# Kernel tuning notes

Measured on AMD Instinct MI355X. Metric: run time of the kernel, lower is better.

The kernel has to match this reference:

```python
import jax, jax.numpy as jnp
import numpy as np
import math

N_HEADS = 16
ROPE_THETA = 10000.0
NEG_INF = -1e30


def setup_inputs() -> dict:
    key = jax.random.key(0)
    k1, k2, k3, k4 = jax.random.split(key, 4)
    B, S, D = 2, 2048, 2048
    x = jax.random.normal(k1, (B, S, D), dtype=jnp.float32)
    qkv = 0.01 * jax.random.normal(k2, (2 * D, D), dtype=jnp.float32)
    H = N_HEADS
    dh = D // H
    nope = dh // 2
    rope = dh // 2
    wk = 0.01 * jax.random.normal(k3, (H * nope + rope, D), dtype=jnp.float32)
    wo = 0.01 * jax.random.normal(k4, (D, D), dtype=jnp.float32)
    return {"x": x, "qkv": qkv, "wk": wk, "wo": wo}


def _rope_cos_sin(S, dh, rope_dim, dtype):
    # freqs over full dh as in the torch module, then sliced to rope_dim//2 and tiled x2
    freqs = 1.0 / (ROPE_THETA ** (jnp.arange(0, dh, 2).astype(jnp.float32) / dh))
    emb = jnp.arange(S, dtype=jnp.float32)[:, None] * freqs[None, :]  # [S, dh//2]
    cos = jnp.tile(jnp.cos(emb)[:, : rope_dim // 2], (1, 2))[None, None]  # [1,1,S,rope]
    sin = jnp.tile(jnp.sin(emb)[:, : rope_dim // 2], (1, 2))[None, None]
    return cos.astype(dtype), sin.astype(dtype)


def _apply_rope(xq, cos, sin):
    x1, x2 = jnp.split(xq, 2, axis=-1)
    return xq * cos + jnp.concatenate([-x2, x1], axis=-1) * sin


def reference(x, qkv, wk, wo):
    B, S, D = x.shape
    H = N_HEADS
    dh = D // H
    nope = dh // 2
    rope = dh // 2

    QV = x @ qkv.T                              # [B,S,2D]
    Q, V = jnp.split(QV, 2, axis=-1)
    Q = Q.reshape(B, S, H, dh).transpose(0, 2, 1, 3)        # [B,H,S,dh]
    v_heads = V.reshape(B, S, H, dh).transpose(0, 2, 1, 3)  # [B,H,S,dh]
    Qn, Qr = Q[..., :nope], Q[..., nope:]

    K = x @ wk.T                                # [B,S,H*nope+rope]
    Kn = K[..., : H * nope].reshape(B, S, H, nope).transpose(0, 2, 1, 3)  # [B,H,S,nope]
    Kr = K[..., H * nope :].reshape(B, S, 1, rope).transpose(0, 2, 1, 3)  # [B,1,S,rope]

    cos, sin = _rope_cos_sin(S, dh, rope, x.dtype)
    Qr = _apply_rope(Qr, cos, sin)
    Kr = _apply_rope(Kr, cos, sin)

    q_heads = jnp.concatenate([Qn, Qr], axis=-1)                               # [B,H,S,dh]
    k_heads = jnp.concatenate([Kn, jnp.broadcast_to(Kr, (B, H, S, rope))], -1)  # [B,H,S,dh]

    scale = 1.0 / math.sqrt(dh)
    scores = jnp.einsum('bhqd,bhkd->bhqk', q_heads, k_heads) * scale
    mask = jnp.tril(jnp.ones((S, S), dtype=bool))
    scores = jnp.where(mask[None, None], scores, NEG_INF)
    attn = jax.nn.softmax(scores, axis=-1)
    out = jnp.einsum('bhqk,bhkd->bhqd', attn, v_heads)
    out = out.transpose(0, 2, 1, 3).reshape(B, S, D) @ wo.T
    return (out, k_heads, v_heads)
```

## Files before the change

### kernel.cpp

```cpp
#include <hip/hip_runtime.h>
#include <hip/hip_bf16.h>


typedef unsigned short u16;
typedef unsigned int u32;
typedef __bf16 bf16x8 __attribute__((ext_vector_type(8)));
typedef float f32x4 __attribute__((ext_vector_type(4)));
typedef float f32x16 __attribute__((ext_vector_type(16)));

__device__ __forceinline__ u16 f2bf(float x) {
  union { __hip_bfloat16 h; u16 u; } c;
  c.h = __float2bfloat16(x);
  return c.u;
}
__device__ __forceinline__ float bf2f(u16 u) {
  union { u32 u; float f; } c;
  c.u = ((u32)u) << 16;
  return c.f;
}
__device__ __forceinline__ u32 pack2(float a, float b) {
  return (u32)f2bf(a) | ((u32)f2bf(b) << 16);
}
__device__ __forceinline__ f32x4 mfma16(bf16x8 a, bf16x8 b, f32x4 c) {
  return __builtin_amdgcn_mfma_f32_16x16x32_bf16(a, b, c, 0, 0, 0);
}
__device__ __forceinline__ f32x16 mfma32(bf16x8 a, bf16x8 b, f32x16 c) {
  return __builtin_amdgcn_mfma_f32_32x32x16_bf16(a, b, c, 0, 0, 0);
}
__device__ __forceinline__ void gload_lds16(const void* g, void* l) {
  __builtin_amdgcn_global_load_lds((__attribute__((address_space(1))) void*)g,
                                   (__attribute__((address_space(3))) void*)l,
                                   16, 0, 0);
}

__global__ __launch_bounds__(256) void cast_all(const float4* __restrict__ x,
                                                const float4* __restrict__ qkv,
                                                const float* __restrict__ wk,
                                                const float4* __restrict__ wo,
                                                u16* __restrict__ x_bf,
                                                u16* __restrict__ wcomb,
                                                u16* __restrict__ wo_bf) {
  int i = blockIdx.x * blockDim.x + threadIdx.x;
  const float4* src;
  u16* dst;
  int j;
  if (i < 2097152) {
    src = x; dst = x_bf; j = i;
  } else if (i < 4194304) {
    src = qkv; dst = wcomb; j = i - 2097152;
  } else if (i < 4849664) {
    j = i - 4194304;
    int r = (j * 4) >> 11;
    u32 lo = 0, hi = 0;
    if (r < 1088) {
      float4 v = ((const float4*)wk)[j];
      lo = pack2(v.x, v.y);
      hi = pack2(v.z, v.w);
    }
    ((uint2*)(wcomb + 8388608))[j] = make_uint2(lo, hi);
    return;
  } else {
    src = wo; dst = wo_bf; j = i - 4849664;
  }
  float4 v = src[j];
  ((uint2*)dst)[j] = make_uint2(pack2(v.x, v.y), pack2(v.z, v.w));
}

__device__ __forceinline__ void cstore(u16* C, size_t i, float v) { C[i] = f2bf(v); }
__device__ __forceinline__ void cstore(float* C, size_t i, float v) { C[i] = v; }

template <typename CT, int BM, int BN>
__global__ __launch_bounds__(512, 2) void gemm256(const u16* __restrict__ A,
                                                  const u16* __restrict__ W,
                                                  CT* __restrict__ C,
                                                  int M, int N, int K) {
  constexpr int MI = BM / 64;
  constexpr int NI = BN / 128;
  constexpr int AH = BM * 64;
  constexpr int BH = BN * 64;
  constexpr int AL = BM / 128;
  constexpr int BL = BN / 128;
  constexpr int BOFF = 4 * AH;
  __shared__ char lds[BOFF + 4 * BH];
  const int tid = threadIdx.x;
  const int wid = tid >> 6, lane = tid & 63;
  const int lr = lane & 15, lg = lane >> 4;
  const int wr = wid >> 2, wc = wid & 3;
  const int xorv = (lr & 7) << 4;
  const int nwg = gridDim.x * gridDim.y;
  const int lin = blockIdx.y * gridDim.x + blockIdx.x;
  const int swz = (lin & 7) * (nwg >> 3) + (lin >> 3);
  const int m0 = (swz / gridDim.x) * BM;
  const int n0 = (swz % gridDim.x) * BN;
  const int nkt = K >> 6;

  f32x4 acc[2 * MI][2 * NI] = {};
  bf16x8 a[MI][2], b[2 * NI][2];

  const int o0 = tid * 16, o1 = 8192 + tid * 16;
  const int r0 = o0 >> 7, c0 = ((o0 & 127) ^ ((r0 & 7) << 4)) >> 1;
  const int r1 = o1 >> 7, c1 = ((o1 & 127) ^ ((r1 & 7) << 4)) >> 1;
  const u16* gA0[2] = {A + (size_t)(m0 + r0) * K + c0,
                       A + (size_t)(m0 + BM / 2 + r0) * K + c0};
  const u16* gA1[2] = {A + (size_t)(m0 + r1) * K + c1,
                       A + (size_t)(m0 + BM / 2 + r1) * K + c1};
  const u16* gB0[2] = {W + (size_t)(n0 + r0) * K + c0,
                       W + (size_t)(n0 + BN / 2 + r0) * K + c0};
  const u16* gB1[2] = {W + (size_t)(n0 + r1) * K + c1,
                       W + (size_t)(n0 + BN / 2 + r1) * K + c1};

  auto STAGEA = [&](int t, int h) {
    char* d_ = lds + (t & 1) * (2 * AH) + h * AH + wid * 1024;
    gload_lds16(gA0[h] + (size_t)t * 64, d_);
    if constexpr (AL == 2) gload_lds16(gA1[h] + (size_t)t * 64, d_ + 8192);
  };
  auto STAGEB = [&](int t, int h) {
    char* d_ = lds + BOFF + (t & 1) * (2 * BH) + h * BH + wid * 1024;
    gload_lds16(gB0[h] + (size_t)t * 64, d_);
    if constexpr (BL == 2) gload_lds16(gB1[h] + (size_t)t * 64, d_ + 8192);
  };
  auto WAITKEEP = [&]() {
    if constexpr (AL + BL == 4) asm volatile("s_waitcnt vmcnt(4)" ::: "memory");
    else asm volatile("s_waitcnt vmcnt(3)" ::: "memory");
  };

  STAGEA(0, 0); STAGEB(0, 0); STAGEA(0, 1); STAGEB(0, 1);
  if (nkt > 1) { STAGEA(1, 0); STAGEB(1, 0); }
  WAITKEEP();
  __builtin_amdgcn_s_barrier();

  for (int t = 0; t < nkt; ++t) {
    const char* Ab = lds + (t & 1) * (2 * AH);
    const char* Bb = lds + BOFF + (t & 1) * (2 * BH);
    const int arow = wr * (BM / 4), brow = wc * (BN / 8);
#pragma unroll
    for (int mi = 0; mi < MI; mi++)
#pragma unroll
      for (int ks = 0; ks < 2; ks++)
        a[mi][ks] = *(const bf16x8*)(Ab + (arow + mi * 16 + lr) * 128 + ((lg * 16 + ks * 64) ^ xorv));
#pragma unroll
    for (int ni = 0; ni < NI; ni++)
#pragma unroll
      for (int ks = 0; ks < 2; ks++)
        b[ni][ks] = *(const bf16x8*)(Bb + (brow + ni * 16 + lr) * 128 + ((lg * 16 + ks * 64) ^ xorv));
    if (t + 1 < nkt) STAGEA(t + 1, 1);
    __builtin_amdgcn_s_barrier();
    asm volatile("s_waitcnt lgkmcnt(0)" ::: "memory");
    __builtin_amdgcn_sched_barrier(0);
    __builtin_amdgcn_s_setprio(1);
#pragma unroll
    for (int mi = 0; mi < MI; mi++)
#pragma unroll
      for (int ni = 0; ni < NI; ni++)
#pragma unroll
        for (int ks = 0; ks < 2; ks++)
          acc[mi][ni] = mfma16(a[mi][ks], b[ni][ks], acc[mi][ni]);
    __builtin_amdgcn_s_setprio(0);
    __builtin_amdgcn_s_barrier();
#pragma unroll
    for (int ni = 0; ni < NI; ni++)
#pragma unroll
      for (int ks = 0; ks < 2; ks++)
        b[NI + ni][ks] = *(const bf16x8*)(Bb + BH + (brow + ni * 16 + lr) * 128 + ((lg * 16 + ks * 64) ^ xorv));
    if (t + 1 < nkt) STAGEB(t + 1, 1);
    __builtin_amdgcn_s_barrier();
    asm volatile("s_waitcnt lgkmcnt(0)" ::: "memory");
    __builtin_amdgcn_sched_barrier(0);
    __builtin_amdgcn_s_setprio(1);
#pragma unroll
    for (int mi = 0; mi < MI; mi++)
#pragma unroll
      for (int ni = 0; ni < NI; ni++)
#pragma unroll
        for (int ks = 0; ks < 2; ks++)
          acc[mi][NI + ni] = mfma16(a[mi][ks], b[NI + ni][ks], acc[mi][NI + ni]);
    __builtin_amdgcn_s_setprio(0);
    __builtin_amdgcn_s_barrier();
#pragma unroll
    for (int mi = 0; mi < MI; mi++)
#pragma unroll
      for (int ks = 0; ks < 2; ks++)
        a[mi][ks] = *(const bf16x8*)(Ab + AH + (arow + mi * 16 + lr) * 128 + ((lg * 16 + ks * 64) ^ xorv));
    if (t + 2 < nkt) STAGEA(t + 2, 0);
    __builtin_amdgcn_s_barrier();
    asm volatile("s_waitcnt lgkmcnt(0)" ::: "memory");
    __builtin_amdgcn_sched_barrier(0);
    __builtin_amdgcn_s_setprio(1);
#pragma unroll
    for (int mi = 0; mi < MI; mi++)
#pragma unroll
      for (int ni = 0; ni < NI; ni++)
#pragma unroll
        for (int ks = 0; ks < 2; ks++)
          acc[MI + mi][ni] = mfma16(a[mi][ks], b[ni][ks], acc[MI + mi][ni]);
    __builtin_amdgcn_s_setprio(0);
    __builtin_amdgcn_s_barrier();
    if (t + 2 < nkt) {
      STAGEB(t + 2, 0);
      WAITKEEP();
    } else if (t + 1 < nkt) {
      asm volatile("s_waitcnt vmcnt(0)" ::: "memory");
    }
    __builtin_amdgcn_s_barrier();
    asm volatile("s_waitcnt lgkmcnt(0)" ::: "memory");
    __builtin_amdgcn_sched_barrier(0);
    __builtin_amdgcn_s_setprio(1);
#pragma unroll
    for (int mi = 0; mi < MI; mi++)
#pragma unroll
      for (int ni = 0; ni < NI; ni++)
#pragma unroll
        for (int ks = 0; ks < 2; ks++)
          acc[MI + mi][NI + ni] = mfma16(a[mi][ks], b[NI + ni][ks], acc[MI + mi][NI + ni]);
    __builtin_amdgcn_s_setprio(0);
    __builtin_amdgcn_s_barrier();
  }

#pragma unroll
  for (int Mh = 0; Mh < 2; Mh++)
#pragma unroll
    for (int mi = 0; mi < MI; mi++) {
      int row = m0 + Mh * (BM / 2) + wr * (BM / 4) + mi * 16 + lg * 4;
#pragma unroll
      for (int Nh = 0; Nh < 2; Nh++)
#pragma unroll
        for (int ni = 0; ni < NI; ni++) {
          int col = n0 + Nh * (BN / 2) + wc * (BN / 8) + ni * 16 + lr;
#pragma unroll
          for (int r = 0; r < 4; r++)
            cstore(C, (size_t)(row + r) * N + col, acc[Mh * MI + mi][Nh * NI + ni][r]);
        }
    }
}

__global__ __launch_bounds__(256) void rope_scatter2(u16* __restrict__ QVK,
                                                     u16* __restrict__ kh,
                                                     float* __restrict__ k_out, int S) {
  const int row = blockIdx.x;
  const int b = row >> 11, s = row & 2047;
  const int tid = threadIdx.x;
  __shared__ float kr[64];
  const float LOG1E4_64 = 0.14391156511f;
  u16* qrow = QVK + (size_t)row * 5376;
  if (tid < 32) {
    float freq = __expf(-(float)tid * LOG1E4_64);
    float sn, c;
    __sincosf((float)s * freq, &sn, &c);
    float a = bf2f(qrow[5120 + tid]);
    float bb = bf2f(qrow[5152 + tid]);
    kr[tid] = a * c - bb * sn;
    kr[tid + 32] = bb * c + a * sn;
  }
  for (int idx = tid; idx < 512; idx += 256) {
    int h = idx >> 5, jj = idx & 31;
    float freq = __expf(-(float)jj * LOG1E4_64);
    float sn, c;
    __sincosf((float)s * freq, &sn, &c);
    u16* p1 = qrow + h * 128 + 64 + jj;
    u16* p2 = qrow + h * 128 + 96 + jj;
    float x1 = bf2f(*p1), x2 = bf2f(*p2);
    *p1 = f2bf(x1 * c - x2 * sn);
    *p2 = f2bf(x2 * c + x1 * sn);
  }
  __syncthreads();
  for (int idx = tid; idx < 2048; idx += 256) {
    int h = idx >> 7, d = idx & 127;
    float val = (d < 64) ? bf2f(qrow[4096 + h * 64 + d]) : kr[d - 64];
    size_t o = ((size_t)(b * 16 + h) * S + s) * 128 + d;
    kh[o] = f2bf(val);
    k_out[o] = val;
  }
}

__global__ __launch_bounds__(256) void v_scatter(const u16* __restrict__ QVK,
                                                 u16* __restrict__ vt,
                                                 float* __restrict__ v_out, int S) {
  const int blk = blockIdx.x;
  const int st = blk & 63;
  const int dt = (blk >> 6) & 3;
  const int bh = blk >> 8;
  const int b = bh >> 4, h = bh & 15;
  __shared__ u16 t[32][34];
  const int tx = threadIdx.x & 31, ty = threadIdx.x >> 5;
  const int s0 = st * 32, d0 = dt * 32;
#pragma unroll
  for (int i = 0; i < 4; i++) {
    int sl = ty + 8 * i;
    u16 u = QVK[(size_t)(b * S + s0 + sl) * 5376 + 2048 + h * 128 + d0 + tx];
    t[sl][tx] = u;
    v_out[((size_t)bh * S + s0 + sl) * 128 + d0 + tx] = bf2f(u);
  }
  __syncthreads();
#pragma unroll
  for (int i = 0; i < 4; i++) {
    int dl = ty + 8 * i;
    vt[((size_t)bh * 128 + d0 + dl) * S + s0 + tx] = t[tx][dl];
  }
}

__global__ __launch_bounds__(256) void flash_attn6(const u16* __restrict__ QVK,
                                                   const u16* __restrict__ Kh,
                                                   const u16* __restrict__ Vt,
                                                   u16* __restrict__ attn, int S) {
  __shared__ char lds[49664];
  const int tid = threadIdx.x, wid = tid >> 6, lane = tid & 63;
  const int bh = blockIdx.x & 31;
  const int qb = 15 - (int)(blockIdx.x >> 5);
  const int q0w = qb * 128 + wid * 32;
  const int b = bh >> 4, h = bh & 15;
  const int r32 = lane & 31, hh = lane >> 5;
  const u16* Qb = QVK + (size_t)b * S * 5376 + h * 128;
  const u16* Kb = Kh + (size_t)bh * S * 128;
  const u16* Vb = Vt + (size_t)bh * 128 * S;
  const int qg = q0w + r32;
  const int xr = (r32 & 7) << 4;
  char* const Pc = lds + 49152 + wid * 128;

  const u16 *srcK[4], *srcV[4];
#pragma unroll
  for (int i = 0; i < 4; i++) {
    int o = i * 4096 + tid * 16;
    int rK = o >> 8, cbK = (o & 255) ^ ((rK & 7) << 4);
    srcK[i] = Kb + rK * 128 + (cbK >> 1);
    int dV = o >> 7, kbV = (o & 127) ^ ((dV & 7) << 4);
    srcV[i] = Vb + (size_t)dV * S + (kbV >> 1);
  }

  bf16x8 qf[8];
#pragma unroll
  for (int f = 0; f < 8; f++)
    qf[f] = *(const bf16x8*)(Qb + (size_t)qg * 5376 + f * 16 + hh * 8);

  f32x16 acc[4] = {};
  float m = -INFINITY, l = 0.f;
  const float sc = 0.08838834764831845f;
  const int ktiles = 2 * qb + 2;

#pragma unroll
  for (int i = 0; i < 4; i++) {
    char* ld = lds + i * 4096 + wid * 1024;
    gload_lds16(srcK[i], ld);
    gload_lds16(srcV[i], ld + 32768);
  }
  asm volatile("s_waitcnt vmcnt(0)" ::: "memory");
  __builtin_amdgcn_s_barrier();

  for (int kt = 0; kt < ktiles; ++kt) {
    const char* Kt = lds + (kt & 1) * 16384;
    const char* Vl = lds + 32768;
    const bool more = (kt + 1 < ktiles);
    if (more) {
#pragma unroll
      for (int i = 0; i < 4; i++)
        gload_lds16(srcK[i] + (size_t)(kt + 1) * 8192,
                    lds + (((kt & 1) ^ 1) << 14) + i * 4096 + wid * 1024);
      asm volatile("s_waitcnt vmcnt(8)" ::: "memory");
    } else {
      asm volatile("s_waitcnt vmcnt(4)" ::: "memory");
    }
    __builtin_amdgcn_s_barrier();

    const int kbg = kt * 64;
    const bool active = (kbg <= q0w + 31);
    u32 u[16];
    if (active) {
      f32x16 s[2] = {};
      __builtin_amdgcn_s_setprio(1);
#pragma unroll
      for (int kg = 0; kg < 2; kg++) {
        const char* Kq = Kt + (kg * 32 + r32) * 256;
#pragma unroll
        for (int f = 0; f < 8; f++) {
          bf16x8 kf = *(const bf16x8*)(Kq + ((f * 32 + hh * 16) ^ xr));
          s[kg] = mfma32(kf, qf[f], s[kg]);
        }
      }
      __builtin_amdgcn_s_setprio(0);
      const bool maskt = (kbg + 63 > q0w);
      if (maskt) {
#pragma unroll
        for (int kg = 0; kg < 2; kg++)
#pragma unroll
          for (int r = 0; r < 16; r++)
            if (kbg + kg * 32 + (r & 3) + 8 * (r >> 2) + 4 * hh > qg)
              s[kg][r] = -1e30f;
      }
      float tm = s[0][0];
#pragma unroll
      for (int r = 1; r < 16; r++) tm = fmaxf(tm, s[0][r]);
#pragma unroll
      for (int r = 0; r < 16; r++) tm = fmaxf(tm, s[1][r]);
      tm = fmaxf(tm, __shfl_xor(tm, 32));
      if (!__all(tm <= m + 64.0f)) {
        float mnew = fmaxf(m, tm);
        float corr = __expf((m - mnew) * sc);
        m = mnew;
        l *= corr;
        if (lane < 32) *(float*)(Pc + r32 * 4) = corr;
        asm volatile("s_waitcnt lgkmcnt(0)" ::: "memory");
        __builtin_amdgcn_sched_barrier(0);
        f32x4 c0 = *(const f32x4*)(Pc + (4 * hh) * 4);
        f32x4 c1 = *(const f32x4*)(Pc + (8 + 4 * hh) * 4);
        f32x4 c2 = *(const f32x4*)(Pc + (16 + 4 * hh) * 4);
        f32x4 c3 = *(const f32x4*)(Pc + (24 + 4 * hh) * 4);
#pragma unroll
        for (int dg = 0; dg < 4; dg++)
#pragma unroll
          for (int r = 0; r < 16; r++) {
            float cr = (r >> 2) == 0 ? c0[r & 3]
                     : (r >> 2) == 1 ? c1[r & 3]
                     : (r >> 2) == 2 ? c2[r & 3] : c3[r & 3];
            acc[dg][r] *= cr;
          }
      }
      const float nms = -m * sc;
      float ts = 0.f;
#pragma unroll
      for (int kg = 0; kg < 2; kg++)
#pragma unroll
        for (int r = 0; r < 16; r++) {
          float pv = __expf(fmaf(s[kg][r], sc, nms));
          s[kg][r] = pv;
          ts += pv;
        }
      ts += __shfl_xor(ts, 32);
      l += ts;
#pragma unroll
      for (int kg = 0; kg < 2; kg++)
#pragma unroll
        for (int i = 0; i < 8; i++)
          u[kg * 8 + i] = pack2(s[kg][2 * i], s[kg][2 * i + 1]);
    }

    if (more) asm volatile("s_waitcnt vmcnt(4)" ::: "memory");
    else      asm volatile("s_waitcnt vmcnt(0)" ::: "memory");
    __builtin_amdgcn_s_barrier();

    if (active) {
      __builtin_amdgcn_s_setprio(1);
#pragma unroll
      for (int dg = 0; dg < 4; dg++) {
        const char* Vq = Vl + (dg * 32 + r32) * 128;
#pragma unroll
        for (int ss = 0; ss < 4; ss++) {
          uint2 vlo = *(const uint2*)(Vq + ((ss * 32 + 8 * hh) ^ xr));
          uint2 vhi = *(const uint2*)(Vq + ((ss * 32 + 16 + 8 * hh) ^ xr));
          union { u32 w[4]; bf16x8 v; } vb, pa;
          vb.w[0] = vlo.x; vb.w[1] = vlo.y; vb.w[2] = vhi.x; vb.w[3] = vhi.y;
          pa.w[0] = u[ss * 4 + 0];
          pa.w[1] = u[ss * 4 + 1];
          pa.w[2] = u[ss * 4 + 2];
          pa.w[3] = u[ss * 4 + 3];
          acc[dg] = mfma32(pa.v, vb.v, acc[dg]);
        }
      }
      __builtin_amdgcn_s_setprio(0);
    }
    __builtin_amdgcn_s_barrier();
    if (more) {
#pragma unroll
      for (int i = 0; i < 4; i++)
        gload_lds16(srcV[i] + (size_t)(kt + 1) * 64,
                    lds + 32768 + i * 4096 + wid * 1024);
    }
  }

  float linv = 1.0f / l;
  if (lane < 32) *(float*)(Pc + r32 * 4) = linv;
  asm volatile("s_waitcnt lgkmcnt(0)" ::: "memory");
  __builtin_amdgcn_sched_barrier(0);
  f32x4 l0 = *(const f32x4*)(Pc + (4 * hh) * 4);
  f32x4 l1 = *(const f32x4*)(Pc + (8 + 4 * hh) * 4);
  f32x4 l2 = *(const f32x4*)(Pc + (16 + 4 * hh) * 4);
  f32x4 l3 = *(const f32x4*)(Pc + (24 + 4 * hh) * 4);
  u16* ab = attn + (size_t)(b * S + q0w) * 2048 + h * 128;
#pragma unroll
  for (int dg = 0; dg < 4; dg++)
#pragma unroll
    for (int r = 0; r < 16; r++) {
      int rowl = (r & 3) + 8 * (r >> 2) + 4 * hh;
      float li = (r >> 2) == 0 ? l0[r & 3]
               : (r >> 2) == 1 ? l1[r & 3]
               : (r >> 2) == 2 ? l2[r & 3] : l3[r & 3];
      ab[(size_t)rowl * 2048 + dg * 32 + r32] = f2bf(acc[dg][r] * li);
    }
}

extern "C" void kernel_launch(void* const* d_in, const int* in_sizes, int n_in,
                              void* d_out, int out_size, void* d_ws, size_t ws_size,
                              hipStream_t stream) {
  (void)in_sizes; (void)n_in; (void)out_size; (void)ws_size;
  const int S = 2048;
  const float* x = (const float*)d_in[0];
  const float* qkv = (const float*)d_in[1];
  const float* wk = (const float*)d_in[2];
  const float* wo = (const float*)d_in[3];
  float* out = (float*)d_out;
  float* k_out = out + (size_t)8388608;
  float* v_out = out + (size_t)16777216;

  char* ws = (char*)d_ws;
  u16* x_bf  = (u16*)(ws + 0);
  u16* wcomb = (u16*)(ws + 16777216);
  u16* wo_bf = (u16*)(ws + 38797312);
  u16* qvk   = (u16*)(ws + 47185920);
  u16* vt_bf = (u16*)(ws + 91226112);
  u16* attn_bf = x_bf;
  u16* k_bf = wcomb;

  cast_all<<<23040, 256, 0, stream>>>((const float4*)x, (const float4*)qkv, wk,
                                      (const float4*)wo, x_bf, wcomb, wo_bf);

  gemm256<u16, 256, 256><<<dim3(16, 16), 512, 0, stream>>>(x_bf, wcomb, qvk,
                                                           4096, 5376, 2048);
  gemm256<u16, 256, 128><<<dim3(10, 16), 512, 0, stream>>>(
      x_bf, wcomb + (size_t)4096 * 2048, qvk + 4096, 4096, 5376, 2048);
  rope_scatter2<<<4096, 256, 0, stream>>>(qvk, k_bf, k_out, S);
  v_scatter<<<8192, 256, 0, stream>>>(qvk, vt_bf, v_out, S);
  flash_attn6<<<512, 256, 0, stream>>>(qvk, k_bf, vt_bf, attn_bf, S);
  gemm256<float, 128, 256><<<dim3(8, 32), 512, 0, stream>>>(attn_bf, wo_bf, out,
                                                            4096, 2048, 2048);
}
```

Before: 275.6 us.

## Stage V tiles through registers instead of direct global-to-LDS loads in flash attention

The next V tile is now prefetched into registers alongside the asynchronous K-tile loads. It is written into LDS after the current tile's compute, between two full barriers. This removes the mid-iteration waitcnt and barrier between the QK^T and PV phases, so the score and PV MFMAs can run back to back. In exchange it costs extra VGPRs for the staged data, explicit LDS store instructions, and a second barrier at the end of each iteration.

```diff
diff --git a/kernel.cpp b/kernel.cpp
--- a/kernel.cpp
+++ b/kernel.cpp
@@ -298,7 +298,7 @@
   }
 }
 
-__global__ __launch_bounds__(256) void flash_attn6(const u16* __restrict__ QVK,
+__global__ __launch_bounds__(256) void flash_attn7(const u16* __restrict__ QVK,
                                                    const u16* __restrict__ Kh,
                                                    const u16* __restrict__ Vt,
                                                    u16* __restrict__ attn, int S) {
@@ -336,14 +336,17 @@
   const float sc = 0.08838834764831845f;
   const int ktiles = 2 * qb + 2;
 
+  uint4 vreg[4];
 #pragma unroll
   for (int i = 0; i < 4; i++) {
-    char* ld = lds + i * 4096 + wid * 1024;
-    gload_lds16(srcK[i], ld);
-    gload_lds16(srcV[i], ld + 32768);
+    gload_lds16(srcK[i], lds + i * 4096 + wid * 1024);
+    vreg[i] = *(const uint4*)srcV[i];
   }
   asm volatile("s_waitcnt vmcnt(0)" ::: "memory");
-  __builtin_amdgcn_s_barrier();
+#pragma unroll
+  for (int i = 0; i < 4; i++)
+    *(uint4*)(lds + 32768 + i * 4096 + tid * 16) = vreg[i];
+  __syncthreads();
 
   for (int kt = 0; kt < ktiles; ++kt) {
     const char* Kt = lds + (kt & 1) * 16384;
@@ -351,19 +354,17 @@
     const bool more = (kt + 1 < ktiles);
     if (more) {
 #pragma unroll
-      for (int i = 0; i < 4; i++)
+      for (int i = 0; i < 4; i++) {
         gload_lds16(srcK[i] + (size_t)(kt + 1) * 8192,
                     lds + (((kt & 1) ^ 1) << 14) + i * 4096 + wid * 1024);
-      asm volatile("s_waitcnt vmcnt(8)" ::: "memory");
-    } else {
-      asm volatile("s_waitcnt vmcnt(4)" ::: "memory");
-    }
-    __builtin_amdgcn_s_barrier();
+        vreg[i] = *(const uint4*)(srcV[i] + (size_t)(kt + 1) * 64);
+      }
+    }
 
     const int kbg = kt * 64;
     const bool active = (kbg <= q0w + 31);
-    u32 u[16];
     if (active) {
+      u32 u[16];
       f32x16 s[2] = {};
       __builtin_amdgcn_s_setprio(1);
 #pragma unroll
@@ -430,13 +431,7 @@
 #pragma unroll
         for (int i = 0; i < 8; i++)
           u[kg * 8 + i] = pack2(s[kg][2 * i], s[kg][2 * i + 1]);
-    }
-
-    if (more) asm volatile("s_waitcnt vmcnt(4)" ::: "memory");
-    else      asm volatile("s_waitcnt vmcnt(0)" ::: "memory");
-    __builtin_amdgcn_s_barrier();
-
-    if (active) {
+
       __builtin_amdgcn_s_setprio(1);
 #pragma unroll
       for (int dg = 0; dg < 4; dg++) {
@@ -456,13 +451,14 @@
       }
       __builtin_amdgcn_s_setprio(0);
     }
-    __builtin_amdgcn_s_barrier();
+
+    __syncthreads();
     if (more) {
 #pragma unroll
       for (int i = 0; i < 4; i++)
-        gload_lds16(srcV[i] + (size_t)(kt + 1) * 64,
-                    lds + 32768 + i * 4096 + wid * 1024);
-    }
+        *(uint4*)(lds + 32768 + i * 4096 + tid * 16) = vreg[i];
+    }
+    __syncthreads();
   }
 
   float linv = 1.0f / l;
@@ -517,7 +513,7 @@
       x_bf, wcomb + (size_t)4096 * 2048, qvk + 4096, 4096, 5376, 2048);
   rope_scatter2<<<4096, 256, 0, stream>>>(qvk, k_bf, k_out, S);
   v_scatter<<<8192, 256, 0, stream>>>(qvk, vt_bf, v_out, S);
-  flash_attn6<<<512, 256, 0, stream>>>(qvk, k_bf, vt_bf, attn_bf, S);
+  flash_attn7<<<512, 256, 0, stream>>>(qvk, k_bf, vt_bf, attn_bf, S);
   gemm256<float, 128, 256><<<dim3(8, 32), 512, 0, stream>>>(attn_bf, wo_bf, out,
                                                             4096, 2048, 2048);
 }
```

After: 301.5 us. 1.09x slower.

## Split long causal attention rows across two blocks and merge partials

Applied to the files above, without the earlier changes.

For the upper half of query blocks (qb>=8), the KV range is split across two blocks, each writing unnormalized bf16 accumulators plus running max and sum to scratch in the output buffer. A new combine kernel rescales the two partials and writes the final attention output. Short query blocks run unsplit as before. This is meant to even out per-block work under the causal mask and raise parallelism from 512 to 768 blocks, at the cost of an extra launch, partial-result traffic, and bf16 rounding of the partials.

```diff
diff --git a/kernel.cpp b/kernel.cpp
--- a/kernel.cpp
+++ b/kernel.cpp
@@ -298,14 +298,30 @@
   }
 }
 
-__global__ __launch_bounds__(256) void flash_attn6(const u16* __restrict__ QVK,
+__global__ __launch_bounds__(256) void flash_attn9(const u16* __restrict__ QVK,
                                                    const u16* __restrict__ Kh,
                                                    const u16* __restrict__ Vt,
-                                                   u16* __restrict__ attn, int S) {
+                                                   u16* __restrict__ attn,
+                                                   u16* __restrict__ accP,
+                                                   float* __restrict__ mP,
+                                                   float* __restrict__ lP, int S) {
   __shared__ char lds[49664];
   const int tid = threadIdx.x, wid = tid >> 6, lane = tid & 63;
-  const int bh = blockIdx.x & 31;
-  const int qb = 15 - (int)(blockIdx.x >> 5);
+  const int j = blockIdx.x;
+  int bh, qb, ktb, kte, pblk;
+  if (j < 512) {
+    qb = 15 - (j >> 6);
+    bh = (j & 63) >> 1;
+    const int half = j & 1;
+    if (half == 0) { ktb = 0; kte = qb + 1; }
+    else { ktb = qb + 1; kte = 2 * qb + 2; }
+    pblk = (bh * 8 + (qb - 8)) * 2 + half;
+  } else {
+    const int jj = j - 512;
+    qb = 7 - (jj >> 5);
+    bh = jj & 31;
+    ktb = 0; kte = 2 * qb + 2; pblk = 0;
+  }
   const int q0w = qb * 128 + wid * 32;
   const int b = bh >> 4, h = bh & 15;
   const int r32 = lane & 31, hh = lane >> 5;
@@ -334,21 +350,20 @@
   f32x16 acc[4] = {};
   float m = -INFINITY, l = 0.f;
   const float sc = 0.08838834764831845f;
-  const int ktiles = 2 * qb + 2;
 
 #pragma unroll
   for (int i = 0; i < 4; i++) {
-    char* ld = lds + i * 4096 + wid * 1024;
-    gload_lds16(srcK[i], ld);
-    gload_lds16(srcV[i], ld + 32768);
+    gload_lds16(srcK[i] + (size_t)ktb * 8192,
+                lds + ((ktb & 1) << 14) + i * 4096 + wid * 1024);
+    gload_lds16(srcV[i] + (size_t)ktb * 64, lds + 32768 + i * 4096 + wid * 1024);
   }
   asm volatile("s_waitcnt vmcnt(0)" ::: "memory");
   __builtin_amdgcn_s_barrier();
 
-  for (int kt = 0; kt < ktiles; ++kt) {
+  for (int kt = ktb; kt < kte; ++kt) {
     const char* Kt = lds + (kt & 1) * 16384;
     const char* Vl = lds + 32768;
-    const bool more = (kt + 1 < ktiles);
+    const bool more = (kt + 1 < kte);
     if (more) {
 #pragma unroll
       for (int i = 0; i < 4; i++)
@@ -465,25 +480,72 @@
     }
   }
 
-  float linv = 1.0f / l;
-  if (lane < 32) *(float*)(Pc + r32 * 4) = linv;
-  asm volatile("s_waitcnt lgkmcnt(0)" ::: "memory");
-  __builtin_amdgcn_sched_barrier(0);
-  f32x4 l0 = *(const f32x4*)(Pc + (4 * hh) * 4);
-  f32x4 l1 = *(const f32x4*)(Pc + (8 + 4 * hh) * 4);
-  f32x4 l2 = *(const f32x4*)(Pc + (16 + 4 * hh) * 4);
-  f32x4 l3 = *(const f32x4*)(Pc + (24 + 4 * hh) * 4);
-  u16* ab = attn + (size_t)(b * S + q0w) * 2048 + h * 128;
-#pragma unroll
-  for (int dg = 0; dg < 4; dg++)
-#pragma unroll
-    for (int r = 0; r < 16; r++) {
-      int rowl = (r & 3) + 8 * (r >> 2) + 4 * hh;
-      float li = (r >> 2) == 0 ? l0[r & 3]
-               : (r >> 2) == 1 ? l1[r & 3]
-               : (r >> 2) == 2 ? l2[r & 3] : l3[r & 3];
-      ab[(size_t)rowl * 2048 + dg * 32 + r32] = f2bf(acc[dg][r] * li);
-    }
+  if (j < 512) {
+    if (lane < 32) {
+      mP[pblk * 128 + wid * 32 + r32] = m;
+      lP[pblk * 128 + wid * 32 + r32] = l;
+    }
+    u16* ap = accP + (size_t)pblk * 16384;
+#pragma unroll
+    for (int dg = 0; dg < 4; dg++)
+#pragma unroll
+      for (int r = 0; r < 16; r++) {
+        int rowl = (r & 3) + 8 * (r >> 2) + 4 * hh;
+        ap[(size_t)(wid * 32 + rowl) * 128 + dg * 32 + r32] = f2bf(acc[dg][r]);
+      }
+  } else {
+    float linv = 1.0f / l;
+    if (lane < 32) *(float*)(Pc + r32 * 4) = linv;
+    asm volatile("s_waitcnt lgkmcnt(0)" ::: "memory");
+    __builtin_amdgcn_sched_barrier(0);
+    f32x4 l0 = *(const f32x4*)(Pc + (4 * hh) * 4);
+    f32x4 l1 = *(const f32x4*)(Pc + (8 + 4 * hh) * 4);
+    f32x4 l2 = *(const f32x4*)(Pc + (16 + 4 * hh) * 4);
+    f32x4 l3 = *(const f32x4*)(Pc + (24 + 4 * hh) * 4);
+    u16* ab = attn + (size_t)(b * S + qb * 128 + wid * 32) * 2048 + h * 128;
+#pragma unroll
+    for (int dg = 0; dg < 4; dg++)
+#pragma unroll
+      for (int r = 0; r < 16; r++) {
+        int rowl = (r & 3) + 8 * (r >> 2) + 4 * hh;
+        float li = (r >> 2) == 0 ? l0[r & 3]
+                 : (r >> 2) == 1 ? l1[r & 3]
+                 : (r >> 2) == 2 ? l2[r & 3] : l3[r & 3];
+        ab[(size_t)rowl * 2048 + dg * 32 + r32] = f2bf(acc[dg][r] * li);
+      }
+  }
+}
+
+__global__ __launch_bounds__(256) void combine_attn(const u16* __restrict__ accP,
+                                                    const float* __restrict__ mP,
+                                                    const float* __restrict__ lP,
+                                                    u16* __restrict__ attn, int S) {
+  const int blk = blockIdx.x;
+  const int bh = blk >> 3, qb = (blk & 7) + 8;
+  const int b = bh >> 4, h = bh & 15;
+  const int tid = threadIdx.x;
+  const float sc = 0.08838834764831845f;
+  __shared__ float w0[128], w1[128];
+  if (tid < 128) {
+    float m0 = mP[(blk * 2) * 128 + tid], m1 = mP[(blk * 2 + 1) * 128 + tid];
+    float l0 = lP[(blk * 2) * 128 + tid], l1 = lP[(blk * 2 + 1) * 128 + tid];
+    float mm = fmaxf(m0, m1);
+    float c0 = __expf((m0 - mm) * sc), c1 = __expf((m1 - mm) * sc);
+    float inv = 1.0f / (c0 * l0 + c1 * l1);
+    w0[tid] = c0 * inv;
+    w1[tid] = c1 * inv;
+  }
+  __syncthreads();
+  const u16* a0 = accP + (size_t)(blk * 2) * 16384;
+  const u16* a1 = a0 + 16384;
+  u16* ab = attn + (size_t)(b * S + qb * 128) * 2048 + h * 128;
+#pragma unroll
+  for (int e = 0; e < 64; e++) {
+    int idx = e * 256 + tid;
+    int q = idx >> 7, d = idx & 127;
+    float v = bf2f(a0[idx]) * w0[q] + bf2f(a1[idx]) * w1[q];
+    ab[(size_t)q * 2048 + d] = f2bf(v);
+  }
 }
 
 extern "C" void kernel_launch(void* const* d_in, const int* in_sizes, int n_in,
@@ -498,6 +560,9 @@
   float* out = (float*)d_out;
   float* k_out = out + (size_t)8388608;
   float* v_out = out + (size_t)16777216;
+  u16* accP = (u16*)d_out;
+  float* mP = (float*)((char*)d_out + 16777216);
+  float* lP = (float*)((char*)d_out + 17039360);
 
   char* ws = (char*)d_ws;
   u16* x_bf  = (u16*)(ws + 0);
@@ -517,7 +582,8 @@
       x_bf, wcomb + (size_t)4096 * 2048, qvk + 4096, 4096, 5376, 2048);
   rope_scatter2<<<4096, 256, 0, stream>>>(qvk, k_bf, k_out, S);
   v_scatter<<<8192, 256, 0, stream>>>(qvk, vt_bf, v_out, S);
-  flash_attn6<<<512, 256, 0, stream>>>(qvk, k_bf, vt_bf, attn_bf, S);
+  flash_attn9<<<768, 256, 0, stream>>>(qvk, k_bf, vt_bf, attn_bf, accP, mP, lP, S);
+  combine_attn<<<256, 256, 0, stream>>>(accP, mP, lP, attn_bf, S);
   gemm256<float, 128, 256><<<dim3(8, 32), 512, 0, stream>>>(attn_bf, wo_bf, out,
                                                             4096, 2048, 2048);
 }
```

Result: slower. 293.0 us (+6.3%).
